# Optimization experiments

Measured on AMD Instinct MI355X. Metric: run time of the kernel, lower is better.

Reference implementation:

```python
import jax, jax.numpy as jnp
import numpy as np
import math

B, TQ, TK, D = 4, 1024, 1024, 1024
H, DK, DV = 16, 64, 64


def _ln(x, g, b, eps=1e-5):
    m = x.mean(-1, keepdims=True)
    v = ((x - m) ** 2).mean(-1, keepdims=True)
    return (x - m) * jax.lax.rsqrt(v + eps) * g + b


def setup_inputs() -> dict:
    key = jax.random.key(0)
    ks = jax.random.split(key, 24)
    s = 0.02
    inp = {
        "x": jax.random.normal(ks[0], (B, TQ, D), jnp.float32),
        "y": jax.random.normal(ks[1], (B, TK, D), jnp.float32),
        "mask": jax.random.randint(ks[2], (B, TK), 0, 2).astype(bool),
        # pre-attention layernorms (affine)
        "ln1_g": jnp.ones((D,)), "ln1_b": jnp.zeros((D,)),
        "ln2_g": jnp.ones((D,)), "ln2_b": jnp.zeros((D,)),
        # mha1 projections
        "q_w": jax.random.normal(ks[3], (D, H * DK)) * s, "q_b": jnp.zeros((H * DK,)),
        "k_w": jax.random.normal(ks[4], (D, H * DK)) * s, "k_b": jnp.zeros((H * DK,)),
        "v_w": jax.random.normal(ks[5], (D, H * DV)) * s, "v_b": jnp.zeros((H * DV,)),
        "o_w": jax.random.normal(ks[6], (H * DV, D)) * s, "o_b": jnp.zeros((D,)),
        # MLP: [LN, ReLU, Linear] x 2 over sizes [D, D, D]
        "mln1_g": jnp.ones((D,)), "mln1_b": jnp.zeros((D,)),
        "l1_w": jax.random.normal(ks[7], (D, D)) * s, "l1_b": jnp.zeros((D,)),
        "mln2_g": jnp.ones((D,)), "mln2_b": jnp.zeros((D,)),
        "l2_w": jax.random.normal(ks[8], (D, D)) * s, "l2_b": jnp.zeros((D,)),
    }
    return inp


def reference(x, y, mask, ln1_g, ln1_b, ln2_g, ln2_b,
              q_w, q_b, k_w, k_b, v_w, v_b, o_w, o_b,
              mln1_g, mln1_b, l1_w, l1_b, mln2_g, mln2_b, l2_w, l2_b):
    # pre-norm + relu
    x1 = jax.nn.relu(_ln(x, ln1_g, ln1_b))
    y1 = jax.nn.relu(_ln(y, ln2_g, ln2_b))
    # cross attention (mha1)
    b, t, _ = x1.shape
    q = (x1 @ q_w + q_b).reshape(b, t, H, DK)
    k = (y1 @ k_w + k_b).reshape(b, -1, H, DK)
    v = (y1 @ v_w + v_b).reshape(b, -1, H, DV)
    logits = jnp.einsum('bthd,bThd->bhtT', q, k) * (1.0 / math.sqrt(DK))
    logits = jnp.where(mask[:, None, None, :], logits, -1e30)
    w = jax.nn.softmax(logits, axis=-1)
    attn = jnp.einsum('bhtT,bThd->bthd', w, v).reshape(b, t, H * DV)
    x = x + (attn @ o_w + o_b)
    # MLP: LN -> ReLU -> Linear, twice
    h = jax.nn.relu(_ln(x, mln1_g, mln1_b)) @ l1_w + l1_b
    out = jax.nn.relu(_ln(h, mln2_g, mln2_b)) @ l2_w + l2_b
    return out
```

## Files before the change

kernel.cpp:

```cpp
#include <hip/hip_runtime.h>
#include <hip/hip_bf16.h>
#include <math.h>

#define D_MODEL 1024
#define NTOK    4096

typedef unsigned short u16;
typedef unsigned int   u32;
typedef __attribute__((ext_vector_type(8))) short  short8;
typedef __attribute__((ext_vector_type(4))) float  floatx4;
typedef __attribute__((ext_vector_type(4))) unsigned short ushort4v;
typedef __attribute__((ext_vector_type(2))) unsigned int   uint2v;

static __host__ __device__ __forceinline__ float bf2f(u16 u) {
    union { unsigned int i; float f; } v; v.i = ((unsigned int)u) << 16; return v.f;
}
static __host__ __device__ __forceinline__ u16 f2bf(float f) {
    union { float f; unsigned int i; } v; v.f = f;
    unsigned int r = (v.i + 0x7FFFu + ((v.i >> 16) & 1u)) >> 16;
    return (u16)r;
}
static __device__ __forceinline__ u32 fbits(float f) {
    union { float f; u32 i; } v; v.f = f; return v.i;
}
static __device__ __forceinline__ void gl2lds16(const void* g, void* l) {
    __builtin_amdgcn_global_load_lds(
        (const __attribute__((address_space(1))) void*)g,
        (__attribute__((address_space(3))) void*)l, 16, 0, 0);
}

__global__ __launch_bounds__(256) void CrossTransformer_27522150432886_kernel(
    float* __restrict__ out, int n, float val)
{
    int i = blockIdx.x * 256 + threadIdx.x;
    if (i < n) out[i] = val;
}

__global__ __launch_bounds__(256) void mask_k(
    const void* __restrict__ mp, float* __restrict__ madd)
{
    const unsigned int* w = (const unsigned int*)mp;
    const int t = threadIdx.x;
    int bad = 0;
    for (int i = t; i < 1024; i += 256) {
        unsigned int v = w[i];
        if (!(v == 0u || v == 1u || v == 0xFFu || v == 0xFFFFFFFFu)) bad++;
    }
#pragma unroll
    for (int off = 32; off > 0; off >>= 1) bad += __shfl_xor(bad, off, 64);
    __shared__ int rb[4];
    if ((t & 63) == 0) rb[t >> 6] = bad;
    __syncthreads();
    const int Bc = rb[0] + rb[1] + rb[2] + rb[3];
    if (Bc * 2 > 1024) {
        const unsigned char* b8 = (const unsigned char*)mp;
        for (int i = t; i < 4096; i += 256) madd[i] = b8[i] ? 0.f : -1e30f;
    } else {
        const int* m32 = (const int*)mp;
        for (int i = t; i < 4096; i += 256) madd[i] = m32[i] ? 0.f : -1e30f;
    }
}

__global__ __launch_bounds__(256) void ln_relu_k(
    const void* __restrict__ in, const float* __restrict__ gam,
    const float* __restrict__ bet, u16* __restrict__ out, int bf16in)
{
    const int row = blockIdx.x, t = threadIdx.x;
    float v0, v1, v2, v3;
    if (bf16in) {
        ushort4v u = *(const ushort4v*)((const u16*)in + (size_t)row * D_MODEL + t * 4);
        v0 = bf2f(u[0]); v1 = bf2f(u[1]); v2 = bf2f(u[2]); v3 = bf2f(u[3]);
    } else {
        const float4 p = *(const float4*)((const float*)in + (size_t)row * D_MODEL + t * 4);
        v0 = p.x; v1 = p.y; v2 = p.z; v3 = p.w;
    }
    float s = v0 + v1 + v2 + v3;
    float q = v0 * v0 + v1 * v1 + v2 * v2 + v3 * v3;
#pragma unroll
    for (int off = 32; off > 0; off >>= 1) {
        s += __shfl_xor(s, off, 64);
        q += __shfl_xor(q, off, 64);
    }
    __shared__ float red[2][4];
    if ((t & 63) == 0) { red[0][t >> 6] = s; red[1][t >> 6] = q; }
    __syncthreads();
    s = red[0][0] + red[0][1] + red[0][2] + red[0][3];
    q = red[1][0] + red[1][1] + red[1][2] + red[1][3];

    const float mean = s * (1.0f / D_MODEL);
    const float var  = q * (1.0f / D_MODEL) - mean * mean;
    const float rstd = rsqrtf(var + 1e-5f);

    const float4 gp = *(const float4*)(gam + t * 4);
    const float4 bp = *(const float4*)(bet + t * 4);
    ushort4v o;
    o[0] = f2bf(fmaxf((v0 - mean) * rstd * gp.x + bp.x, 0.f));
    o[1] = f2bf(fmaxf((v1 - mean) * rstd * gp.y + bp.y, 0.f));
    o[2] = f2bf(fmaxf((v2 - mean) * rstd * gp.z + bp.z, 0.f));
    o[3] = f2bf(fmaxf((v3 - mean) * rstd * gp.w + bp.w, 0.f));
    *(ushort4v*)(out + (size_t)row * D_MODEL + t * 4) = o;
}

struct W6 { const float* w[6]; };
__global__ __launch_bounds__(256) void wtrans_k(W6 wp, u16* __restrict__ WtBase)
{
    __shared__ u16 tile[32][33];
    const float* W  = wp.w[blockIdx.z];
    u16*         Wt = WtBase + (size_t)blockIdx.z * D_MODEL * D_MODEL;
    const int c0 = blockIdx.x * 32, r0 = blockIdx.y * 32;
    const int tx = threadIdx.x, ty = threadIdx.y;
#pragma unroll
    for (int j = 0; j < 4; j++)
        tile[ty + j * 8][tx] = f2bf(W[(size_t)(r0 + ty + j * 8) * D_MODEL + c0 + tx]);
    __syncthreads();
#pragma unroll
    for (int j = 0; j < 4; j++)
        Wt[(size_t)(c0 + ty + j * 8) * D_MODEL + r0 + tx] = tile[tx][ty + j * 8];
}

struct GB {
    const u16* A; const u16* Bt; const float* bias; const float* resid;
    u16* C; float* Cf; float scale; int vt;
};
struct GB3 { GB g[3]; u16* VtG; };

__global__ __launch_bounds__(256) void gemm_qkv_k(GB3 gb)
{
    const GB cfg = gb.g[blockIdx.z];
    __shared__ __align__(16) u16 sm[16384];
    u16* As = sm; u16* Bs = sm + 4096;
    const int t = threadIdx.x, lane = t & 63, w = t >> 6;
    const int wy = w >> 1, wx = w & 1;
    const int bm = blockIdx.y * 128, bn = blockIdx.x * 128;
    const int m = lane & 15, g = lane >> 4;
    const int arow = t >> 2, aseg = (t & 3) * 8;

    floatx4 acc[4][4] = {};
    for (int k0 = 0; k0 < D_MODEL; k0 += 32) {
#pragma unroll
        for (int i = 0; i < 2; i++) {
            gl2lds16(cfg.A  + (size_t)(bm + i * 64 + arow) * D_MODEL + k0 + aseg,
                     (char*)As + i * 4096 + w * 1024);
            gl2lds16(cfg.Bt + (size_t)(bn + i * 64 + arow) * D_MODEL + k0 + aseg,
                     (char*)Bs + i * 4096 + w * 1024);
        }
        __syncthreads();
        short8 af[4], bf[4];
#pragma unroll
        for (int mt = 0; mt < 4; mt++)
            af[mt] = *(const short8*)(As + (wy * 64 + mt * 16 + m) * 32 + g * 8);
#pragma unroll
        for (int nt = 0; nt < 4; nt++)
            bf[nt] = *(const short8*)(Bs + (wx * 64 + nt * 16 + m) * 32 + g * 8);
#pragma unroll
        for (int mt = 0; mt < 4; mt++)
#pragma unroll
            for (int nt = 0; nt < 4; nt++)
                acc[mt][nt] = __builtin_amdgcn_mfma_f32_16x16x32_bf16(
                    af[mt], bf[nt], acc[mt][nt], 0, 0, 0);
        __syncthreads();
    }

    float bv[4];
#pragma unroll
    for (int nt = 0; nt < 4; nt++)
        bv[nt] = cfg.bias[bn + wx * 64 + nt * 16 + m];

    if (!cfg.vt) {
#pragma unroll
        for (int mt = 0; mt < 4; mt++)
#pragma unroll
            for (int r = 0; r < 4; r++) {
                const int grow = bm + wy * 64 + mt * 16 + g * 4 + r;
#pragma unroll
                for (int nt = 0; nt < 4; nt++) {
                    const int col = bn + wx * 64 + nt * 16 + m;
                    float val = (acc[mt][nt][r] + bv[nt]) * cfg.scale;
                    cfg.C[(size_t)grow * D_MODEL + col] = f2bf(val);
                }
            }
    } else {
        u16* Lt = sm;
        const int b16  = (bm >> 10) * 16;
        const int bn6  = bn >> 6;
        const int tok0 = bm & 1023;
#pragma unroll
        for (int hh = 0; hh < 2; hh++) {
            if (wx == hh) {
#pragma unroll
                for (int mt = 0; mt < 4; mt++)
#pragma unroll
                    for (int r = 0; r < 4; r++) {
                        const int tok = wy * 64 + mt * 16 + g * 4 + r;
#pragma unroll
                        for (int nt = 0; nt < 4; nt++) {
                            const int d = nt * 16 + m;
                            Lt[d * 128 + (((tok >> 3) ^ (d & 15)) << 3) + (tok & 7)] =
                                f2bf(acc[mt][nt][r] + bv[nt]);
                        }
                    }
            }
            __syncthreads();
#pragma unroll
            for (int j = 0; j < 4; j++) {
                const int s = j * 256 + t;
                const int d = s >> 4, c = s & 15;
                short8 v = *(const short8*)(Lt + d * 128 + ((c ^ (d & 15)) << 3));
                *(short8*)(gb.VtG + ((size_t)((b16 + bn6 + hh) * 64 + d)) * 1024 + tok0 + c * 8) = v;
            }
            __syncthreads();
        }
    }
}

__global__ __launch_bounds__(256) void gemm_k(GB3 gb)
{
    const GB cfg = gb.g[blockIdx.z];
    __shared__ __align__(16) u16 sm[8192];
    u16* As = sm; u16* Bs = sm + 4096;
    const int t = threadIdx.x, lane = t & 63, w = t >> 6;
    const int wy = w >> 1, wx = w & 1;
    const int bm = blockIdx.y * 128, bn = blockIdx.x * 64;
    const int m = lane & 15, g = lane >> 4;
    const int arow = (lane >> 2), aseg = (lane & 3) * 8;

    floatx4 acc[4][2] = {};
    for (int k0 = 0; k0 < D_MODEL; k0 += 32) {
#pragma unroll
        for (int i = 0; i < 2; i++)
            gl2lds16(cfg.A + (size_t)(bm + i * 64 + w * 16 + arow) * D_MODEL + k0 + aseg,
                     (char*)As + i * 4096 + w * 1024);
        gl2lds16(cfg.Bt + (size_t)(bn + w * 16 + arow) * D_MODEL + k0 + aseg,
                 (char*)Bs + w * 1024);
        __syncthreads();
        short8 af[4], bf[2];
#pragma unroll
        for (int mt = 0; mt < 4; mt++)
            af[mt] = *(const short8*)(As + (wy * 64 + mt * 16 + m) * 32 + g * 8);
#pragma unroll
        for (int nt = 0; nt < 2; nt++)
            bf[nt] = *(const short8*)(Bs + (wx * 32 + nt * 16 + m) * 32 + g * 8);
#pragma unroll
        for (int mt = 0; mt < 4; mt++)
#pragma unroll
            for (int nt = 0; nt < 2; nt++)
                acc[mt][nt] = __builtin_amdgcn_mfma_f32_16x16x32_bf16(
                    af[mt], bf[nt], acc[mt][nt], 0, 0, 0);
        __syncthreads();
    }

    float bv[2]; int cols[2];
#pragma unroll
    for (int nt = 0; nt < 2; nt++) {
        cols[nt] = bn + wx * 32 + nt * 16 + m;
        bv[nt]   = cfg.bias[cols[nt]];
    }
#pragma unroll
    for (int mt = 0; mt < 4; mt++) {
#pragma unroll
        for (int r = 0; r < 4; r++) {
            const int grow = bm + wy * 64 + mt * 16 + g * 4 + r;
#pragma unroll
            for (int nt = 0; nt < 2; nt++) {
                float val = (acc[mt][nt][r] + bv[nt]) * cfg.scale;
                if (cfg.resid) val += cfg.resid[(size_t)grow * D_MODEL + cols[nt]];
                if (cfg.Cf) cfg.Cf[(size_t)grow * D_MODEL + cols[nt]] = val;
                else        cfg.C [(size_t)grow * D_MODEL + cols[nt]] = f2bf(val);
            }
        }
    }
}

__global__ __launch_bounds__(256) void attn_k(
    const u16* __restrict__ Q, const u16* __restrict__ Kk,
    const u16* __restrict__ VtG, const float* __restrict__ maddG,
    u16* __restrict__ Ob)
{
    __shared__ __align__(16) char smraw[41472];
    u16*   Ks   = (u16*)smraw;
    u16*   Vt   = (u16*)(smraw + 9216);
    u16*   Ps   = (u16*)(smraw + 18432);
    float* madd = (float*)(smraw + 36864);
    float* liS  = (float*)(smraw + 40960);

    const int qt = blockIdx.x, h = blockIdx.y, b = blockIdx.z;
    const int t = threadIdx.x, lane = t & 63, w = t >> 6;
    const int m = lane & 15, g = lane >> 4;

    for (int i = t; i < 1024; i += 256) madd[i] = maddG[b * 1024 + i];

    short8 qf[2][2];
    const u16* Qb = Q + ((size_t)(b * 1024 + qt * 128 + w * 32 + m)) * D_MODEL + h * 64 + g * 8;
#pragma unroll
    for (int q2 = 0; q2 < 2; q2++)
#pragma unroll
        for (int hf = 0; hf < 2; hf++)
            qf[q2][hf] = *(const short8*)(Qb + q2 * 16 * D_MODEL + hf * 32);

    u16* Pw = Ps + w * 32 * 72;
    const u16* Kp = Kk  + (size_t)(b * 1024) * D_MODEL + h * 64;
    const u16* Vp = VtG + (size_t)((b * 16 + h) * 64) * 1024;

    floatx4 Ov[2][4] = {};
    float li[2] = { 0.f, 0.f };

    for (int kt = 0; kt < 1024; kt += 64) {
#pragma unroll
        for (int i = 0; i < 2; i++) {
            const int s = i * 256 + t, row = s >> 3, seg = (s & 7) * 8;
            *(short8*)(Ks + row * 72 + seg) =
                *(const short8*)(Kp + (size_t)(kt + row) * D_MODEL + seg);
            *(short8*)(Vt + row * 72 + seg) =
                *(const short8*)(Vp + (size_t)row * 1024 + kt + seg);
        }
        __syncthreads();

        short8 af[4][2];
        float4 md[4];
#pragma unroll
        for (int tile = 0; tile < 4; tile++) {
            af[tile][0] = *(const short8*)(Ks + (tile * 16 + m) * 72 + g * 8);
            af[tile][1] = *(const short8*)(Ks + (tile * 16 + m) * 72 + 32 + g * 8);
            md[tile]    = *(const float4*)(madd + kt + tile * 16 + g * 4);
        }

#pragma unroll
        for (int q2 = 0; q2 < 2; q2++) {
            floatx4 st[4];
#pragma unroll
            for (int tile = 0; tile < 4; tile++) {
                floatx4 z = {};
                z = __builtin_amdgcn_mfma_f32_16x16x32_bf16(af[tile][0], qf[q2][0], z, 0, 0, 0);
                st[tile] = __builtin_amdgcn_mfma_f32_16x16x32_bf16(af[tile][1], qf[q2][1], z, 0, 0, 0);
            }
            float rs = 0.f;
#pragma unroll
            for (int tile = 0; tile < 4; tile++) {
                float p0 = exp2f(st[tile][0] + md[tile].x);
                float p1 = exp2f(st[tile][1] + md[tile].y);
                float p2 = exp2f(st[tile][2] + md[tile].z);
                float p3 = exp2f(st[tile][3] + md[tile].w);
                rs += (p0 + p1) + (p2 + p3);
                uint2v pk;
                pk[0] = __builtin_amdgcn_perm(fbits(p1), fbits(p0), 0x07060302u);
                pk[1] = __builtin_amdgcn_perm(fbits(p3), fbits(p2), 0x07060302u);
                *(uint2v*)(Pw + (q2 * 16 + m) * 72 + tile * 16 + g * 4) = pk;
            }
            rs += __shfl_xor(rs, 16, 64);
            rs += __shfl_xor(rs, 32, 64);
            li[q2] += rs;
        }

        short8 pa[2][2], vb[4][2];
#pragma unroll
        for (int q2 = 0; q2 < 2; q2++) {
            pa[q2][0] = *(const short8*)(Pw + (q2 * 16 + m) * 72 + g * 8);
            pa[q2][1] = *(const short8*)(Pw + (q2 * 16 + m) * 72 + 32 + g * 8);
        }
#pragma unroll
        for (int nt = 0; nt < 4; nt++) {
            vb[nt][0] = *(const short8*)(Vt + (nt * 16 + m) * 72 + g * 8);
            vb[nt][1] = *(const short8*)(Vt + (nt * 16 + m) * 72 + 32 + g * 8);
        }
#pragma unroll
        for (int q2 = 0; q2 < 2; q2++)
#pragma unroll
            for (int nt = 0; nt < 4; nt++) {
                Ov[q2][nt] = __builtin_amdgcn_mfma_f32_16x16x32_bf16(
                    pa[q2][0], vb[nt][0], Ov[q2][nt], 0, 0, 0);
                Ov[q2][nt] = __builtin_amdgcn_mfma_f32_16x16x32_bf16(
                    pa[q2][1], vb[nt][1], Ov[q2][nt], 0, 0, 0);
            }
        __syncthreads();
    }

    if (g == 0) { liS[w * 32 + m] = li[0]; liS[w * 32 + 16 + m] = li[1]; }
    __builtin_amdgcn_s_waitcnt(0);
    float4 inv4[2];
#pragma unroll
    for (int q2 = 0; q2 < 2; q2++) {
        float4 l4 = *(const float4*)(liS + w * 32 + q2 * 16 + g * 4);
        inv4[q2].x = 1.0f / fmaxf(l4.x, 1e-37f);
        inv4[q2].y = 1.0f / fmaxf(l4.y, 1e-37f);
        inv4[q2].z = 1.0f / fmaxf(l4.z, 1e-37f);
        inv4[q2].w = 1.0f / fmaxf(l4.w, 1e-37f);
    }
#pragma unroll
    for (int q2 = 0; q2 < 2; q2++) {
        const float iv[4] = { inv4[q2].x, inv4[q2].y, inv4[q2].z, inv4[q2].w };
#pragma unroll
        for (int nt = 0; nt < 4; nt++)
#pragma unroll
            for (int r = 0; r < 4; r++) {
                const int tok = qt * 128 + w * 32 + q2 * 16 + g * 4 + r;
                Ob[(size_t)(b * 1024 + tok) * D_MODEL + h * 64 + nt * 16 + m] =
                    f2bf(Ov[q2][nt][r] * iv[r]);
            }
    }
}

extern "C" __attribute__((visibility("default")))
void kernel_launch(void* const* d_in, const int* in_sizes, int n_in,
                   void* d_out, int out_size, void* d_ws, size_t ws_size,
                   hipStream_t stream)
{
    (void)in_sizes; (void)n_in;
    const float* x      = (const float*)d_in[0];
    const float* y      = (const float*)d_in[1];
    const void*  maskp  = d_in[2];
    const float* ln1_g  = (const float*)d_in[3];
    const float* ln1_b  = (const float*)d_in[4];
    const float* ln2_g  = (const float*)d_in[5];
    const float* ln2_b  = (const float*)d_in[6];
    const float* q_w    = (const float*)d_in[7];
    const float* q_b    = (const float*)d_in[8];
    const float* k_w    = (const float*)d_in[9];
    const float* k_b    = (const float*)d_in[10];
    const float* v_w    = (const float*)d_in[11];
    const float* v_b    = (const float*)d_in[12];
    const float* o_w    = (const float*)d_in[13];
    const float* o_b    = (const float*)d_in[14];
    const float* mln1_g = (const float*)d_in[15];
    const float* mln1_b = (const float*)d_in[16];
    const float* l1_w   = (const float*)d_in[17];
    const float* l1_b   = (const float*)d_in[18];
    const float* mln2_g = (const float*)d_in[19];
    const float* mln2_b = (const float*)d_in[20];
    const float* l2_w   = (const float*)d_in[21];
    const float* l2_b   = (const float*)d_in[22];

    const int nout = out_size;
    const size_t MB = 1024 * 1024;
    if (ws_size < 61 * MB) {
        CrossTransformer_27522150432886_kernel<<<(nout + 255) / 256, 256, 0, stream>>>(
            (float*)d_out, nout, 7.0f);
        return;
    }

    char* ws = (char*)d_ws;
    const size_t WE = (size_t)D_MODEL * D_MODEL;
    u16*   wt   = (u16*)(ws);
    u16*   xn   = (u16*)(ws + 12 * MB);
    u16*   yn   = (u16*)(ws + 20 * MB);
    u16*   Qb   = (u16*)(ws + 28 * MB);
    u16*   Kb   = (u16*)(ws + 36 * MB);
    u16*   VtG  = (u16*)(ws + 44 * MB);
    u16*   attn = (u16*)(ws + 52 * MB);
    float* madd = (float*)(ws + 60 * MB);
    u16* x2 = xn; u16* m1n = Qb; u16* hb = Kb; u16* m2n = VtG;

    mask_k<<<1, 256, 0, stream>>>(maskp, madd);

    W6 wp; wp.w[0] = q_w; wp.w[1] = k_w; wp.w[2] = v_w;
    wp.w[3] = o_w; wp.w[4] = l1_w; wp.w[5] = l2_w;
    wtrans_k<<<dim3(32, 32, 6), dim3(32, 8), 0, stream>>>(wp, wt);

    ln_relu_k<<<NTOK, 256, 0, stream>>>(x, ln1_g, ln1_b, xn, 0);
    ln_relu_k<<<NTOK, 256, 0, stream>>>(y, ln2_g, ln2_b, yn, 0);

    const float qscale = 0.18033688011112042f;
    GB3 qkv = {};
    qkv.g[0] = GB{ xn, wt + 0 * WE, q_b, nullptr, Qb, nullptr, qscale, 0 };
    qkv.g[1] = GB{ yn, wt + 1 * WE, k_b, nullptr, Kb, nullptr, 1.0f,  0 };
    qkv.g[2] = GB{ yn, wt + 2 * WE, v_b, nullptr, nullptr, nullptr, 1.0f, 1 };
    qkv.VtG = VtG;
    gemm_qkv_k<<<dim3(8, 32, 3), 256, 0, stream>>>(qkv);

    attn_k<<<dim3(8, 16, 4), 256, 0, stream>>>(Qb, Kb, VtG, madd, attn);

    GB3 go = {};
    go.g[0] = GB{ attn, wt + 3 * WE, o_b, x, x2, nullptr, 1.0f, 0 };
    gemm_k<<<dim3(16, 32, 1), 256, 0, stream>>>(go);

    ln_relu_k<<<NTOK, 256, 0, stream>>>(x2, mln1_g, mln1_b, m1n, 1);

    GB3 g1 = {};
    g1.g[0] = GB{ m1n, wt + 4 * WE, l1_b, nullptr, hb, nullptr, 1.0f, 0 };
    gemm_k<<<dim3(16, 32, 1), 256, 0, stream>>>(g1);

    ln_relu_k<<<NTOK, 256, 0, stream>>>(hb, mln2_g, mln2_b, m2n, 1);

    GB3 g2 = {};
    g2.g[0] = GB{ m2n, wt + 5 * WE, l2_b, nullptr, nullptr, (float*)d_out, 1.0f, 0 };
    gemm_k<<<dim3(16, 32, 1), 256, 0, stream>>>(g2);
}
```

Before: 324.2 us.

## Triple-buffer LDS staging in QKV and generic GEMMs with prefetch distance two

Replaces the load-sync-compute-sync loop in both GEMM kernels with a three-stage LDS ring: tiles are prefetched two k-steps ahead via direct global-to-LDS loads, and vmcnt waits plus raw barriers replace __syncthreads so global latency overlaps MFMA work. It also raises wave priority around the MFMA block. The cost is more LDS per block, which may reduce occupancy. The wrapped prefetch at the tail issues redundant loads, and correctness depends on the hand-counted vmcnt thresholds.

```diff
diff --git a/kernel.cpp b/kernel.cpp
--- a/kernel.cpp
+++ b/kernel.cpp
@@ -127,24 +127,41 @@
 __global__ __launch_bounds__(256) void gemm_qkv_k(GB3 gb)
 {
     const GB cfg = gb.g[blockIdx.z];
-    __shared__ __align__(16) u16 sm[16384];
-    u16* As = sm; u16* Bs = sm + 4096;
+    __shared__ __align__(16) u16 sm[3 * 8192];
     const int t = threadIdx.x, lane = t & 63, w = t >> 6;
     const int wy = w >> 1, wx = w & 1;
     const int bm = blockIdx.y * 128, bn = blockIdx.x * 128;
     const int m = lane & 15, g = lane >> 4;
     const int arow = t >> 2, aseg = (t & 3) * 8;
 
+    const u16* Ag = cfg.A  + (size_t)(bm + arow) * D_MODEL + aseg;
+    const u16* Bg = cfg.Bt + (size_t)(bn + arow) * D_MODEL + aseg;
+
+    auto stage = [&](int k0, int s) {
+        char* dst = (char*)sm + s * 16384;
+#pragma unroll
+        for (int i = 0; i < 2; i++) {
+            gl2lds16(Ag + (size_t)(i * 64) * D_MODEL + k0, dst + i * 4096 + w * 1024);
+            gl2lds16(Bg + (size_t)(i * 64) * D_MODEL + k0, dst + 8192 + i * 4096 + w * 1024);
+        }
+    };
+
     floatx4 acc[4][4] = {};
-    for (int k0 = 0; k0 < D_MODEL; k0 += 32) {
-#pragma unroll
-        for (int i = 0; i < 2; i++) {
-            gl2lds16(cfg.A  + (size_t)(bm + i * 64 + arow) * D_MODEL + k0 + aseg,
-                     (char*)As + i * 4096 + w * 1024);
-            gl2lds16(cfg.Bt + (size_t)(bn + i * 64 + arow) * D_MODEL + k0 + aseg,
-                     (char*)Bs + i * 4096 + w * 1024);
-        }
-        __syncthreads();
+    const int NT = D_MODEL / 32;
+
+    stage(0, 0);
+    stage(32, 1);
+    asm volatile("s_waitcnt vmcnt(4)" ::: "memory");
+    __builtin_amdgcn_s_barrier();
+
+    int sb = 0;
+    for (int tt = 0; tt < NT; ++tt) {
+        int tp = tt + 2; if (tp >= NT) tp -= NT;
+        int sbp = sb + 2; if (sbp >= 3) sbp -= 3;
+        stage(tp * 32, sbp);
+
+        const u16* As = sm + sb * 8192;
+        const u16* Bs = As + 4096;
         short8 af[4], bf[4];
 #pragma unroll
         for (int mt = 0; mt < 4; mt++)
@@ -152,14 +169,22 @@
 #pragma unroll
         for (int nt = 0; nt < 4; nt++)
             bf[nt] = *(const short8*)(Bs + (wx * 64 + nt * 16 + m) * 32 + g * 8);
+
+        __builtin_amdgcn_s_setprio(1);
 #pragma unroll
         for (int mt = 0; mt < 4; mt++)
 #pragma unroll
             for (int nt = 0; nt < 4; nt++)
                 acc[mt][nt] = __builtin_amdgcn_mfma_f32_16x16x32_bf16(
                     af[mt], bf[nt], acc[mt][nt], 0, 0, 0);
-        __syncthreads();
-    }
+        __builtin_amdgcn_s_setprio(0);
+
+        asm volatile("s_waitcnt vmcnt(4)" ::: "memory");
+        __builtin_amdgcn_s_barrier();
+        sb = sb + 1; if (sb >= 3) sb -= 3;
+    }
+    asm volatile("s_waitcnt vmcnt(0)" ::: "memory");
+    __builtin_amdgcn_s_barrier();
 
     float bv[4];
 #pragma unroll
@@ -216,23 +241,39 @@
 __global__ __launch_bounds__(256) void gemm_k(GB3 gb)
 {
     const GB cfg = gb.g[blockIdx.z];
-    __shared__ __align__(16) u16 sm[8192];
-    u16* As = sm; u16* Bs = sm + 4096;
+    __shared__ __align__(16) u16 sm[3 * 6144];
     const int t = threadIdx.x, lane = t & 63, w = t >> 6;
     const int wy = w >> 1, wx = w & 1;
     const int bm = blockIdx.y * 128, bn = blockIdx.x * 64;
     const int m = lane & 15, g = lane >> 4;
-    const int arow = (lane >> 2), aseg = (lane & 3) * 8;
+
+    const u16* Ag = cfg.A  + (size_t)(bm + (t >> 2)) * D_MODEL + (t & 3) * 8;
+    const u16* Bg = cfg.Bt + (size_t)(bn + w * 16 + (lane >> 2)) * D_MODEL + (lane & 3) * 8;
+
+    auto stage = [&](int k0, int s) {
+        char* dst = (char*)sm + s * 12288;
+#pragma unroll
+        for (int i = 0; i < 2; i++)
+            gl2lds16(Ag + (size_t)(i * 64) * D_MODEL + k0, dst + i * 4096 + w * 1024);
+        gl2lds16(Bg + k0, dst + 8192 + w * 1024);
+    };
 
     floatx4 acc[4][2] = {};
-    for (int k0 = 0; k0 < D_MODEL; k0 += 32) {
-#pragma unroll
-        for (int i = 0; i < 2; i++)
-            gl2lds16(cfg.A + (size_t)(bm + i * 64 + w * 16 + arow) * D_MODEL + k0 + aseg,
-                     (char*)As + i * 4096 + w * 1024);
-        gl2lds16(cfg.Bt + (size_t)(bn + w * 16 + arow) * D_MODEL + k0 + aseg,
-                 (char*)Bs + w * 1024);
-        __syncthreads();
+    const int NT = D_MODEL / 32;
+
+    stage(0, 0);
+    stage(32, 1);
+    asm volatile("s_waitcnt vmcnt(3)" ::: "memory");
+    __builtin_amdgcn_s_barrier();
+
+    int sb = 0;
+    for (int tt = 0; tt < NT; ++tt) {
+        int tp = tt + 2; if (tp >= NT) tp -= NT;
+        int sbp = sb + 2; if (sbp >= 3) sbp -= 3;
+        stage(tp * 32, sbp);
+
+        const u16* As = sm + sb * 6144;
+        const u16* Bs = As + 4096;
         short8 af[4], bf[2];
 #pragma unroll
         for (int mt = 0; mt < 4; mt++)
@@ -240,14 +281,21 @@
 #pragma unroll
         for (int nt = 0; nt < 2; nt++)
             bf[nt] = *(const short8*)(Bs + (wx * 32 + nt * 16 + m) * 32 + g * 8);
+
+        __builtin_amdgcn_s_setprio(1);
 #pragma unroll
         for (int mt = 0; mt < 4; mt++)
 #pragma unroll
             for (int nt = 0; nt < 2; nt++)
                 acc[mt][nt] = __builtin_amdgcn_mfma_f32_16x16x32_bf16(
                     af[mt], bf[nt], acc[mt][nt], 0, 0, 0);
-        __syncthreads();
-    }
+        __builtin_amdgcn_s_setprio(0);
+
+        asm volatile("s_waitcnt vmcnt(3)" ::: "memory");
+        __builtin_amdgcn_s_barrier();
+        sb = sb + 1; if (sb >= 3) sb -= 3;
+    }
+    asm volatile("s_waitcnt vmcnt(0)" ::: "memory");
 
     float bv[2]; int cols[2];
 #pragma unroll
```

Measured after the change: 309.4 us. 1.05x faster.
